# Kernel optimization log

Hardware: AMD Instinct MI355X
Metric: run time of the kernel (lower is better)

## Reference

```python
import jax, jax.numpy as jnp
import numpy as np

L, D, H, G = 3, 64, 4, 64            # layers, hidden_dim, heads, num_graphs
N, E = 20000, 320000                  # nodes, edges
HD = H * D                            # heads * out_channels = 256
DENSE = 256
EPS = 1e-5


def setup_inputs() -> dict:
    key = jax.random.key(0)
    ks = jax.random.split(key, 32)
    s = 0.05
    f32 = jnp.float32
    inp = {
        "x": jax.random.normal(ks[0], (N, D), f32),
        "edge_attr": jax.random.normal(ks[1], (E, D), f32),
        "edge_index": jax.random.randint(ks[2], (2, E), 0, N, dtype=jnp.int32),
        "batch": ((jnp.arange(N, dtype=jnp.int32) * G) // N).astype(jnp.int32),
        # per-layer TransformerConv params (stacked over layer dim)
        "Wq": jax.random.normal(ks[3], (L, D, HD), f32) * s,
        "bq": jnp.zeros((L, HD), f32),
        "Wk": jax.random.normal(ks[4], (L, D, HD), f32) * s,
        "bk": jnp.zeros((L, HD), f32),
        "Wv": jax.random.normal(ks[5], (L, D, HD), f32) * s,
        "bv": jnp.zeros((L, HD), f32),
        "We": jax.random.normal(ks[6], (L, D, HD), f32) * s,   # lin_edge (no bias in PyG)
        "Wskip": jax.random.normal(ks[7], (L, D, HD), f32) * s,
        "bskip": jnp.zeros((L, HD), f32),
        "bn_gamma": jnp.ones((L, HD), f32),
        "bn_beta": jnp.zeros((L, HD), f32),
        "Wt": jax.random.normal(ks[8], (L, HD, D), f32) * s,   # transf_layers
        "bt": jnp.zeros((L, D), f32),
        # MLP head
        "W1": jax.random.normal(ks[9], (2 * D, DENSE), f32) * s,
        "b1": jnp.zeros((DENSE,), f32),
        "W2": jax.random.normal(ks[10], (DENSE, DENSE // 2), f32) * s,
        "b2": jnp.zeros((DENSE // 2,), f32),
        "W3": jax.random.normal(ks[11], (DENSE // 2, 1), f32) * s,
        "b3": jnp.zeros((1,), f32),
    }
    return inp


def _transformer_conv(x, edge_attr, src, dst, Wq, bq, Wk, bk, Wv, bv, We, Wskip, bskip):
    # PyG TransformerConv, concat=True, beta=False, root_weight=True, eval (no attn dropout)
    q = (x @ Wq + bq).reshape(N, H, D)[dst]                 # [E,H,C]
    k = (x @ Wk + bk).reshape(N, H, D)[src]                 # [E,H,C]
    v = (x @ Wv + bv).reshape(N, H, D)[src]                 # [E,H,C]
    e = (edge_attr @ We).reshape(E, H, D)                   # [E,H,C]
    k = k + e
    logits = (q * k).sum(-1) / jnp.sqrt(jnp.asarray(D, x.dtype))  # [E,H]
    m = jax.ops.segment_max(logits, dst, num_segments=N)    # stable softmax per dst node
    p = jnp.exp(logits - m[dst])
    z = jax.ops.segment_sum(p, dst, num_segments=N)
    w = p / z[dst]                                          # [E,H]
    msg = w[..., None] * (v + e)                            # [E,H,C]
    agg = jax.ops.segment_sum(msg, dst, num_segments=N).reshape(N, HD)
    return agg + x @ Wskip + bskip                          # [N, H*C]


def _batchnorm(h, gamma, beta):
    mu = h.mean(0)
    var = h.var(0)  # biased, as torch BN uses for normalization
    return (h - mu) * jax.lax.rsqrt(var + EPS) * gamma + beta


def reference(x, edge_attr, edge_index, batch, Wq, bq, Wk, bk, Wv, bv, We, Wskip,
              bskip, bn_gamma, bn_beta, Wt, bt, W1, b1, W2, b2, W3, b3):
    src, dst = edge_index[0], edge_index[1]
    counts = jax.ops.segment_sum(jnp.ones((N,), x.dtype), batch, num_segments=G)
    rep = jnp.zeros((G, 2 * D), x.dtype)
    for i in range(L):
        h = _transformer_conv(x, edge_attr, src, dst, Wq[i], bq[i], Wk[i], bk[i],
                              Wv[i], bv[i], We[i], Wskip[i], bskip[i])
        h = _batchnorm(h, bn_gamma[i], bn_beta[i])
        x = jax.nn.relu(h @ Wt[i] + bt[i])                  # [N, D]
        gmx = jax.ops.segment_max(x, batch, num_segments=G)
        gav = jax.ops.segment_sum(x, batch, num_segments=G) / counts[:, None]
        rep = rep + jnp.concatenate([gmx, gav], axis=1)     # sum of per-layer reps
    out = jax.nn.relu(rep @ W1 + b1)
    out = jax.nn.relu(out @ W2 + b2)
    return out @ W3 + b3                                    # [G, 1]
```

## Files before the change

### kernel.cpp

```cpp
#include <hip/hip_runtime.h>
#include <math.h>
#include <float.h>

#define N_NODES 20000
#define N_PAD 20032
#define N_EDGES 320000
#define NGRAPH 64
#define NLAYER 3
#define BN_EPS 1e-5f

typedef short bf16x8 __attribute__((ext_vector_type(8)));
typedef float f32x4 __attribute__((ext_vector_type(4)));
typedef unsigned short u16x8 __attribute__((ext_vector_type(8)));

__device__ inline unsigned short f2bf(float f) {
    unsigned int u = __float_as_uint(f);
    unsigned int r = u + 0x7FFF + ((u >> 16) & 1);
    return (unsigned short)(r >> 16);
}
__device__ inline float bf2f(unsigned short s) {
    return __uint_as_float((unsigned int)s << 16);
}

__global__ void count_kernel(const int* __restrict__ ei, int* __restrict__ cnt) {
    int e = blockIdx.x * blockDim.x + threadIdx.x;
    if (e < N_EDGES) atomicAdd(&cnt[ei[N_EDGES + e]], 1);
}

__global__ void scan_kernel(const int* __restrict__ cnt, int* __restrict__ rowptr) {
    __shared__ int sh[256];
    int t = threadIdx.x;
    const int CH = (N_NODES + 255) / 256;
    int base = t * CH;
    int s = 0;
    for (int i = 0; i < CH; i++) { int idx = base + i; if (idx < N_NODES) s += cnt[idx]; }
    sh[t] = s;
    __syncthreads();
    for (int off = 1; off < 256; off <<= 1) {
        int v = sh[t];
        int add = (t >= off) ? sh[t - off] : 0;
        __syncthreads();
        sh[t] = v + add;
        __syncthreads();
    }
    int run = sh[t] - s;
    for (int i = 0; i < CH; i++) {
        int idx = base + i;
        if (idx < N_NODES) { rowptr[idx] = run; run += cnt[idx]; }
    }
    if (t == 255) rowptr[N_NODES] = sh[255];
}

__global__ void fill_kernel(const int* __restrict__ ei, const int* __restrict__ rowptr,
                            int* __restrict__ cur, int* __restrict__ eidx,
                            int* __restrict__ esrc) {
    int e = blockIdx.x * blockDim.x + threadIdx.x;
    if (e < N_EDGES) {
        int dst = ei[N_EDGES + e];
        int pos = atomicAdd(&cur[dst], 1);
        int slot = rowptr[dst] + pos;
        eidx[slot] = e;
        esrc[slot] = ei[e];
    }
}

__global__ void permute_ea_b_kernel(const float* __restrict__ edge_attr,
                                    const int* __restrict__ eidx,
                                    unsigned short* __restrict__ eaPb) {
    int idx = blockIdx.x * blockDim.x + threadIdx.x;
    if (idx < N_EDGES * 16) {
        int j = idx >> 4, c4 = idx & 15;
        float4 v = *(const float4*)(edge_attr + (size_t)eidx[j] * 64 + c4 * 4);
        ((ushort4*)eaPb)[idx] = make_ushort4(f2bf(v.x), f2bf(v.y), f2bf(v.z), f2bf(v.w));
    }
}

__global__ void wallt2_kernel(const float* __restrict__ Wq, const float* __restrict__ Wk,
                              const float* __restrict__ Wv, const float* __restrict__ Ws,
                              const float* __restrict__ We,
                              const float* __restrict__ bq, const float* __restrict__ bk,
                              const float* __restrict__ bv, const float* __restrict__ bs,
                              unsigned short* __restrict__ WallT, float* __restrict__ ball) {
    int c = blockIdx.x, l = blockIdx.y, k = threadIdx.x;
    int seg = c >> 8, ci = c & 255;
    if (seg < 4) {
        const float* W; const float* b;
        switch (seg) {
            case 0:  W = Wq; b = bq; break;
            case 1:  W = Wk; b = bk; break;
            case 2:  W = Wv; b = bv; break;
            default: W = Ws; b = bs; break;
        }
        WallT[(size_t)l * 81920 + c * 64 + k] = f2bf(W[l * 16384 + k * 256 + ci]);
        if (k == 0) ball[l * 1280 + c] = b[l * 256 + ci];
    } else {
        int h = ci >> 6, d = ci & 63;
        const float* Wql = Wq + l * 16384;
        const float* Wel = We + l * 16384;
        float acc = 0.f;
        for (int cc = 0; cc < 64; cc++)
            acc += Wql[k * 256 + h * 64 + cc] * Wel[d * 256 + h * 64 + cc];
        WallT[(size_t)l * 81920 + c * 64 + k] = f2bf(acc);
        if (k == 0) {
            const float* bql = bq + l * 256;
            float ab = 0.f;
            for (int cc = 0; cc < 64; cc++) ab += bql[h * 64 + cc] * Wel[d * 256 + h * 64 + cc];
            ball[l * 1280 + c] = ab;
        }
    }
}

__global__ void xtobf_kernel(const float* __restrict__ x, unsigned short* __restrict__ xbf) {
    int i4 = blockIdx.x * 256 + threadIdx.x;
    if (i4 >= N_PAD * 64 / 4) return;
    int n = i4 >> 4;
    ushort4 o;
    if (n < N_NODES) {
        float4 v = ((const float4*)x)[i4];
        o = make_ushort4(f2bf(v.x), f2bf(v.y), f2bf(v.z), f2bf(v.w));
    } else o = make_ushort4(0, 0, 0, 0);
    ((ushort4*)xbf)[i4] = o;
}

__global__ __launch_bounds__(256) void gemm_qkvsu3_kernel(
    const unsigned short* __restrict__ xbf,
    const unsigned short* __restrict__ WallT,
    const float* __restrict__ ball,
    unsigned short* __restrict__ qbf, unsigned short* __restrict__ kvbf,
    unsigned short* __restrict__ sbf, unsigned short* __restrict__ ubf) {
    int t = threadIdx.x, wid = t >> 6, lane = t & 63;
    int lrow = lane & 15, lk = lane >> 4;

    bf16x8 bfrag[2][4][2];
    float bias[2][4];
    unsigned short* outp[2]; int ostr[2], mul[2], obase[2];
#pragma unroll
    for (int cg = 0; cg < 2; cg++) {
        int ys = blockIdx.y * 2 + cg;
        int col0 = ys * 64;
        int q = ys & 3;
        if (ys < 4)       { outp[cg] = qbf;  ostr[cg] = 256; mul[cg] = 1; obase[cg] = q * 64; }
        else if (ys < 8)  { outp[cg] = kvbf; ostr[cg] = 512; mul[cg] = 2; obase[cg] = q * 128; }
        else if (ys < 12) { outp[cg] = kvbf; ostr[cg] = 512; mul[cg] = 2; obase[cg] = q * 128 + 1; }
        else if (ys < 16) { outp[cg] = sbf;  ostr[cg] = 256; mul[cg] = 1; obase[cg] = q * 64; }
        else              { outp[cg] = ubf;  ostr[cg] = 256; mul[cg] = 1; obase[cg] = q * 64; }
#pragma unroll
        for (int ct = 0; ct < 4; ct++) {
#pragma unroll
            for (int kc = 0; kc < 2; kc++)
                bfrag[cg][ct][kc] = *(const bf16x8*)(WallT +
                    (size_t)(col0 + ct * 16 + lrow) * 64 + kc * 32 + lk * 8);
            bias[cg][ct] = ball[col0 + ct * 16 + lrow];
        }
    }

    for (int nc = blockIdx.x; nc < N_PAD / 64; nc += gridDim.x) {
        int n0 = nc * 64 + wid * 16;
        bf16x8 a0 = *(const bf16x8*)(xbf + (size_t)(n0 + lrow) * 64 + lk * 8);
        bf16x8 a1 = *(const bf16x8*)(xbf + (size_t)(n0 + lrow) * 64 + 32 + lk * 8);
#pragma unroll
        for (int cg = 0; cg < 2; cg++) {
#pragma unroll
            for (int ct = 0; ct < 4; ct++) {
                f32x4 acc = {bias[cg][ct], bias[cg][ct], bias[cg][ct], bias[cg][ct]};
                acc = __builtin_amdgcn_mfma_f32_16x16x32_bf16(a0, bfrag[cg][ct][0], acc, 0, 0, 0);
                acc = __builtin_amdgcn_mfma_f32_16x16x32_bf16(a1, bfrag[cg][ct][1], acc, 0, 0, 0);
                int cl = ct * 16 + lrow;
#pragma unroll
                for (int r = 0; r < 4; r++) {
                    int n = n0 + lk * 4 + r;
                    if (n < N_NODES)
                        outp[cg][(size_t)n * ostr[cg] + obase[cg] + cl * mul[cg]] = f2bf(acc[r]);
                }
            }
        }
    }
}

__global__ __launch_bounds__(256) void attn8_kernel(
    const unsigned short* __restrict__ eaPb,
    const float* __restrict__ ea_f32,
    const int* __restrict__ eaidx,
    const int* __restrict__ rowptr, const int* __restrict__ esrc,
    const unsigned short* __restrict__ qbf, const unsigned short* __restrict__ ubf,
    const unsigned short* __restrict__ kvbf,
    const unsigned short* __restrict__ sbf,
    unsigned short* __restrict__ hskb,
    unsigned short* __restrict__ raccb) {
    int t = threadIdx.x;
    int wid = t >> 6, lane = t & 63;
    int c4 = lane * 4;
    int ec4 = (lane & 15) * 4;
    for (int n = blockIdx.x * 4 + wid; n < N_NODES; n += gridDim.x * 4) {
        ushort4 qu = *(const ushort4*)(qbf + (size_t)n * 256 + c4);
        ushort4 uu = *(const ushort4*)(ubf + (size_t)n * 256 + c4);
        float4 q4 = make_float4(bf2f(qu.x), bf2f(qu.y), bf2f(qu.z), bf2f(qu.w));
        float4 u4 = make_float4(bf2f(uu.x), bf2f(uu.y), bf2f(uu.z), bf2f(uu.w));
        int j0 = rowptr[n];
        int cnt = rowptr[n + 1] - j0;
        float l = 0.f;
        float4 a4 = make_float4(0.f, 0.f, 0.f, 0.f), r4 = a4;
        u16x8 kvA = {0, 0, 0, 0, 0, 0, 0, 0}, kvB = kvA;
        float4 eA = make_float4(0.f, 0.f, 0.f, 0.f), eB = eA;

#define LOADE(KV, EV, JJ) do { \
        int _j = j0 + (JJ); \
        int _s = __builtin_amdgcn_readfirstlane(esrc[_j]); \
        KV = *(const u16x8*)(kvbf + (size_t)_s * 512 + c4 * 2); \
        if (eaPb) { ushort4 _e = *(const ushort4*)(eaPb + (size_t)_j * 64 + ec4); \
                    EV = make_float4(bf2f(_e.x), bf2f(_e.y), bf2f(_e.z), bf2f(_e.w)); } \
        else { EV = *(const float4*)(ea_f32 + (size_t)eaidx[_j] * 64 + ec4); } \
    } while (0)

#define PROC(KV, EV) do { \
        float p = q4.x * bf2f(KV[0]) + q4.y * bf2f(KV[2]) \
                + q4.z * bf2f(KV[4]) + q4.w * bf2f(KV[6]) \
                + u4.x * EV.x + u4.y * EV.y + u4.z * EV.z + u4.w * EV.w; \
        p += __shfl_xor(p, 1); p += __shfl_xor(p, 2); \
        p += __shfl_xor(p, 4); p += __shfl_xor(p, 8); \
        p = __expf(p * 0.125f); \
        l += p; \
        a4.x += p * bf2f(KV[1]); a4.y += p * bf2f(KV[3]); \
        a4.z += p * bf2f(KV[5]); a4.w += p * bf2f(KV[7]); \
        r4.x += p * EV.x; r4.y += p * EV.y; r4.z += p * EV.z; r4.w += p * EV.w; \
    } while (0)

        if (cnt > 0) LOADE(kvA, eA, 0);
        if (cnt > 1) LOADE(kvB, eB, 1);
        int jj = 0;
        for (; jj + 1 < cnt; jj += 2) {
            u16x8 kv0 = kvA; float4 e0 = eA;
            if (jj + 2 < cnt) LOADE(kvA, eA, jj + 2);
            PROC(kv0, e0);
            u16x8 kv1 = kvB; float4 e1 = eB;
            if (jj + 3 < cnt) LOADE(kvB, eB, jj + 3);
            PROC(kv1, e1);
        }
        if (jj < cnt) PROC(kvA, eA);
#undef LOADE
#undef PROC
        float inv = (l > 0.f) ? 1.f / l : 0.f;
        ushort4 su = *(const ushort4*)(sbf + (size_t)n * 256 + c4);
        *(ushort4*)(hskb + (size_t)n * 256 + c4) = make_ushort4(
            f2bf(a4.x * inv + bf2f(su.x)), f2bf(a4.y * inv + bf2f(su.y)),
            f2bf(a4.z * inv + bf2f(su.z)), f2bf(a4.w * inv + bf2f(su.w)));
        *(ushort4*)(raccb + (size_t)n * 256 + c4) = make_ushort4(
            f2bf(r4.x * inv), f2bf(r4.y * inv), f2bf(r4.z * inv), f2bf(r4.w * inv));
    }
}

__global__ __launch_bounds__(256) void msgbn2_kernel(
    const unsigned short* __restrict__ raccb, const float* __restrict__ We,
    const unsigned short* __restrict__ hskb, unsigned short* __restrict__ hbf,
    float* __restrict__ statsL) {
    int t = threadIdx.x;
    float wcol[64];
#pragma unroll
    for (int d = 0; d < 64; d++) wcol[d] = We[d * 256 + t];
    int hoff = t & 192;
    float s = 0.f, s2 = 0.f;
    for (int n = blockIdx.x * 4; n < N_NODES; n += gridDim.x * 4) {
#pragma unroll
        for (int ni = 0; ni < 4; ni++) {
            const unsigned short* rrow = raccb + (size_t)(n + ni) * 256 + hoff;
            float acc = 0.f;
#pragma unroll
            for (int d4 = 0; d4 < 64; d4 += 4) {
                ushort4 r4 = *(const ushort4*)(rrow + d4);
                acc += bf2f(r4.x) * wcol[d4] + bf2f(r4.y) * wcol[d4 + 1]
                     + bf2f(r4.z) * wcol[d4 + 2] + bf2f(r4.w) * wcol[d4 + 3];
            }
            float hv = bf2f(hskb[(size_t)(n + ni) * 256 + t]) + acc;
            hbf[(size_t)(n + ni) * 256 + t] = f2bf(hv);
            s += hv; s2 += hv * hv;
        }
    }
    int base = (blockIdx.x & 7) * 512;
    atomicAdd(&statsL[base + t], s);
    atomicAdd(&statsL[base + 256 + t], s2);
}

__global__ __launch_bounds__(256) void bn_fold5_kernel(
    const float* __restrict__ statsL,
    const float* __restrict__ gamma, const float* __restrict__ beta,
    const float* __restrict__ Wt, const float* __restrict__ bt,
    unsigned short* __restrict__ WtpT,
    float* __restrict__ biasp) {
    __shared__ float aL[256], bbL[256], part[256];
    int t = threadIdx.x;
    float sum = 0.f, sq = 0.f;
#pragma unroll
    for (int s = 0; s < 8; s++) {
        sum += statsL[s * 512 + t];
        sq  += statsL[s * 512 + 256 + t];
    }
    float mean = sum * (1.f / N_NODES);
    float var = sq * (1.f / N_NODES) - mean * mean;
    float a = rsqrtf(var + BN_EPS) * gamma[t];
    aL[t] = a;
    bbL[t] = beta[t] - mean * a;
    __syncthreads();
    int i0 = blockIdx.x * 2048;
    for (int i = i0 + t; i < i0 + 2048; i += 256) {
        int k = i >> 6, o = i & 63;
        WtpT[o * 256 + k] = f2bf(aL[k] * Wt[i]);
    }
    if (blockIdx.x == 0) {
        float p = 0.f;
        int o = t & 63, kq = (t >> 6) * 64;
        for (int kk = kq; kk < kq + 64; kk++) p += bbL[kk] * Wt[kk * 64 + o];
        part[t] = p;
        __syncthreads();
        if (t < 64) biasp[t] = bt[t] + part[t] + part[64 + t] + part[128 + t] + part[192 + t];
    }
}

__global__ __launch_bounds__(256) void xform4_kernel(
    const unsigned short* __restrict__ hbf,
    const unsigned short* __restrict__ WtpT,
    const float* __restrict__ biasp,
    unsigned short* __restrict__ xbf,
    float* __restrict__ poolmx, float* __restrict__ poolsm, int layer) {
    __shared__ float xt[64][65];
    __shared__ float red[4][2][2][64];
    int t = threadIdx.x, wid = t >> 6, lane = t & 63;
    int lrow = lane & 15, lk = lane >> 4;
    bf16x8 bfrag[4][8];
#pragma unroll
    for (int ct = 0; ct < 4; ct++)
#pragma unroll
        for (int kc = 0; kc < 8; kc++)
            bfrag[ct][kc] = *(const bf16x8*)(WtpT +
                (size_t)(ct * 16 + lrow) * 256 + kc * 32 + lk * 8);
    float bias[4];
#pragma unroll
    for (int ct = 0; ct < 4; ct++) bias[ct] = biasp[ct * 16 + lrow];

    for (int nc = blockIdx.x; nc < N_PAD / 64; nc += gridDim.x) {
        int n0 = nc * 64;
        int nw = n0 + wid * 16;
        f32x4 acc[4];
#pragma unroll
        for (int ct = 0; ct < 4; ct++)
            acc[ct] = {bias[ct], bias[ct], bias[ct], bias[ct]};
#pragma unroll
        for (int kc = 0; kc < 8; kc++) {
            bf16x8 a = *(const bf16x8*)(hbf + (size_t)(nw + lrow) * 256 + kc * 32 + lk * 8);
#pragma unroll
            for (int ct = 0; ct < 4; ct++)
                acc[ct] = __builtin_amdgcn_mfma_f32_16x16x32_bf16(a, bfrag[ct][kc], acc[ct], 0, 0, 0);
        }
#pragma unroll
        for (int ct = 0; ct < 4; ct++) {
            int c = ct * 16 + lrow;
#pragma unroll
            for (int r = 0; r < 4; r++) {
                int n = nw + lk * 4 + r;
                float v = fmaxf(acc[ct][r], 0.f);
                xt[wid * 16 + lk * 4 + r][c] = v;
                if (n < N_NODES) xbf[(size_t)n * 64 + c] = f2bf(v);
            }
        }
        __syncthreads();
        int g0 = (n0 * 64) / 20000;
        int b = ((20000 * (g0 + 1) + 63) >> 6) - n0;
        if (b > 64) b = 64;
        {
            int ch = t & 63, rp = t >> 6;
            float mx0 = 0.f, sm0 = 0.f, mx1 = 0.f, sm1 = 0.f;
            for (int r = rp * 16; r < rp * 16 + 16; r++) {
                if (n0 + r < N_NODES) {
                    float v = xt[r][ch];
                    if (r < b) { mx0 = fmaxf(mx0, v); sm0 += v; }
                    else       { mx1 = fmaxf(mx1, v); sm1 += v; }
                }
            }
            red[rp][0][0][ch] = mx0; red[rp][0][1][ch] = sm0;
            red[rp][1][0][ch] = mx1; red[rp][1][1][ch] = sm1;
        }
        __syncthreads();
        if (t < 128) {
            int seg = t >> 6, ch = t & 63;
            float m = red[0][seg][0][ch], s = red[0][seg][1][ch];
#pragma unroll
            for (int w = 1; w < 4; w++) {
                m = fmaxf(m, red[w][seg][0][ch]);
                s += red[w][seg][1][ch];
            }
            int g = g0 + seg;
            bool valid = (seg == 0) || (b < 64 && g < NGRAPH);
            if (valid) {
                atomicMax((unsigned int*)&poolmx[(layer * NGRAPH + g) * 64 + ch],
                          __float_as_uint(m));
                atomicAdd(&poolsm[(layer * NGRAPH + g) * 64 + ch], s);
            }
        }
        __syncthreads();
    }
}

__global__ __launch_bounds__(256) void head_kernel(
    const float* __restrict__ poolmx, const float* __restrict__ poolsm,
    const float* __restrict__ W1, const float* __restrict__ b1,
    const float* __restrict__ W2, const float* __restrict__ b2,
    const float* __restrict__ W3, const float* __restrict__ b3,
    float* __restrict__ out) {
    int g = blockIdx.x, t = threadIdx.x;
    __shared__ float repL[128], o1sh[256], o2sh[128];
    if (t < 128) {
        int d = t & 63;
        int start = (N_NODES * g + 63) >> 6;
        int end = (N_NODES * (g + 1) + 63) >> 6;
        float v = 0.f;
        if (t < 64) {
#pragma unroll
            for (int l = 0; l < NLAYER; l++) v += poolmx[(l * NGRAPH + g) * 64 + d];
        } else {
            float inv = 1.f / (float)(end - start);
#pragma unroll
            for (int l = 0; l < NLAYER; l++) v += poolsm[(l * NGRAPH + g) * 64 + d] * inv;
        }
        repL[t] = v;
    }
    __syncthreads();
    float a1 = b1[t];
    for (int k = 0; k < 128; k++) a1 += repL[k] * W1[k * 256 + t];
    o1sh[t] = fmaxf(a1, 0.f);
    __syncthreads();
    if (t < 128) {
        float a2 = b2[t];
        for (int k = 0; k < 256; k++) a2 += o1sh[k] * W2[k * 128 + t];
        o2sh[t] = fmaxf(a2, 0.f);
    }
    __syncthreads();
    if (t < 64) {
        float p = o2sh[t] * W3[t] + o2sh[t + 64] * W3[t + 64];
#pragma unroll
        for (int off = 32; off; off >>= 1) p += __shfl_xor(p, off);
        if (t == 0) out[g] = p + b3[0];
    }
}

extern "C" void kernel_launch(void* const* d_in, const int* in_sizes, int n_in,
                              void* d_out, int out_size, void* d_ws, size_t ws_size,
                              hipStream_t stream) {
    const float* x         = (const float*)d_in[0];
    const float* edge_attr = (const float*)d_in[1];
    const int*   ei        = (const int*)d_in[2];
    const float* Wq  = (const float*)d_in[4];
    const float* bq  = (const float*)d_in[5];
    const float* Wk  = (const float*)d_in[6];
    const float* bk  = (const float*)d_in[7];
    const float* Wv  = (const float*)d_in[8];
    const float* bv  = (const float*)d_in[9];
    const float* We  = (const float*)d_in[10];
    const float* Wsk = (const float*)d_in[11];
    const float* bsk = (const float*)d_in[12];
    const float* gam = (const float*)d_in[13];
    const float* bet = (const float*)d_in[14];
    const float* Wt  = (const float*)d_in[15];
    const float* bt  = (const float*)d_in[16];
    const float* W1  = (const float*)d_in[17];
    const float* b1  = (const float*)d_in[18];
    const float* W2  = (const float*)d_in[19];
    const float* b2  = (const float*)d_in[20];
    const float* W3  = (const float*)d_in[21];
    const float* b3  = (const float*)d_in[22];
    float* out = (float*)d_out;

    char* ws = (char*)d_ws;
    size_t off = 0;
    auto alloc = [&](size_t bytes) -> char* {
        char* p = ws + off;
        off += (bytes + 255) & ~(size_t)255;
        return p;
    };
    int*   rowptr = (int*)alloc((N_NODES + 1) * sizeof(int));
    int*   eidx   = (int*)alloc((size_t)N_EDGES * sizeof(int));
    int*   esrc   = (int*)alloc(((size_t)N_EDGES + 16) * sizeof(int));
    unsigned short* qbf  = (unsigned short*)alloc((size_t)N_NODES * 256 * 2);
    unsigned short* kvbf = (unsigned short*)alloc((size_t)N_NODES * 512 * 2);
    unsigned short* sbf  = (unsigned short*)alloc((size_t)N_NODES * 256 * 2);
    unsigned short* ubf  = (unsigned short*)alloc((size_t)N_NODES * 256 * 2);
    unsigned short* hskb = (unsigned short*)alloc((size_t)N_NODES * 256 * 2);
    unsigned short* raccb= (unsigned short*)alloc((size_t)N_NODES * 256 * 2);
    unsigned short* hbf  = (unsigned short*)alloc((size_t)N_PAD * 256 * 2);
    unsigned short* xbf  = (unsigned short*)alloc((size_t)N_PAD * 64 * 2);
    unsigned short* WtpT = (unsigned short*)alloc(64 * 256 * 2);
    float* biasp  = (float*)alloc(64 * sizeof(float));
    unsigned short* WallT = (unsigned short*)alloc((size_t)NLAYER * 81920 * 2);
    float* ball   = (float*)alloc((size_t)NLAYER * 1280 * sizeof(float));
    size_t zero_off = off;
    int*   cur1   = (int*)alloc(N_NODES * sizeof(int));
    int*   cur2   = (int*)alloc(N_NODES * sizeof(int));
    float* statsA = (float*)alloc((size_t)NLAYER * 8 * 512 * sizeof(float));
    float* poolmx = (float*)alloc((size_t)NLAYER * NGRAPH * 64 * sizeof(float));
    float* poolsm = (float*)alloc((size_t)NLAYER * NGRAPH * 64 * sizeof(float));
    size_t zero_bytes = off - zero_off;
    unsigned short* eaPb = (unsigned short*)alloc((size_t)N_EDGES * 64 * 2);
    bool perm = (off <= ws_size);

    hipMemsetAsync(ws + zero_off, 0, zero_bytes, stream);

    count_kernel<<<(N_EDGES + 255) / 256, 256, 0, stream>>>(ei, cur1);
    scan_kernel<<<1, 256, 0, stream>>>(cur1, rowptr);
    fill_kernel<<<(N_EDGES + 255) / 256, 256, 0, stream>>>(ei, rowptr, cur2, eidx, esrc);
    if (perm) {
        permute_ea_b_kernel<<<(N_EDGES * 16 + 255) / 256, 256, 0, stream>>>(
            edge_attr, eidx, eaPb);
    }

    wallt2_kernel<<<dim3(1280, NLAYER), 64, 0, stream>>>(
        Wq, Wk, Wv, Wsk, We, bq, bk, bv, bsk, WallT, ball);
    xtobf_kernel<<<(N_PAD * 64 / 4 + 255) / 256, 256, 0, stream>>>(x, xbf);

    for (int i = 0; i < NLAYER; i++) {
        gemm_qkvsu3_kernel<<<dim3(79, 10), 256, 0, stream>>>(
            xbf, WallT + (size_t)i * 81920, ball + i * 1280, qbf, kvbf, sbf, ubf);

        attn8_kernel<<<5000, 256, 0, stream>>>(
            perm ? eaPb : (const unsigned short*)nullptr, edge_attr,
            eidx, rowptr, esrc, qbf, ubf, kvbf, sbf, hskb, raccb);

        msgbn2_kernel<<<1250, 256, 0, stream>>>(
            raccb, We + i * 16384, hskb, hbf, statsA + (size_t)i * 4096);

        bn_fold5_kernel<<<8, 256, 0, stream>>>(
            statsA + (size_t)i * 4096, gam + i * 256, bet + i * 256,
            Wt + i * 16384, bt + i * 64, WtpT, biasp);

        xform4_kernel<<<157, 256, 0, stream>>>(
            hbf, WtpT, biasp, xbf, poolmx, poolsm, i);
    }

    head_kernel<<<64, 256, 0, stream>>>(poolmx, poolsm, W1, b1, W2, b2, W3, b3, out);
}
```

Measured before the change: 663.3 us.

## Store K/V in fp8 and fuse BN fold into xform kernel

The QKV GEMM now writes the gathered K and V tensors as interleaved fp8 bytes instead of bf16, and the attention kernel decodes them with fp8 conversion intrinsics. This halves the bytes per random gather in the edge loop, at the cost of lower precision in the attention logits and values. The separate BN-fold launch is folded into the xform kernel, where each block recomputes the scale, bias and scaled weight fragments itself. This removes one launch per layer but repeats that small amount of work in every block. The attention grid is also halved.

```diff
diff --git a/kernel.cpp b/kernel.cpp
--- a/kernel.cpp
+++ b/kernel.cpp
@@ -11,7 +11,6 @@
 
 typedef short bf16x8 __attribute__((ext_vector_type(8)));
 typedef float f32x4 __attribute__((ext_vector_type(4)));
-typedef unsigned short u16x8 __attribute__((ext_vector_type(8)));
 
 __device__ inline unsigned short f2bf(float f) {
     unsigned int u = __float_as_uint(f);
@@ -122,28 +121,29 @@
     ((ushort4*)xbf)[i4] = o;
 }
 
-__global__ __launch_bounds__(256) void gemm_qkvsu3_kernel(
+__global__ __launch_bounds__(256) void gemm_qkvsu4_kernel(
     const unsigned short* __restrict__ xbf,
     const unsigned short* __restrict__ WallT,
     const float* __restrict__ ball,
-    unsigned short* __restrict__ qbf, unsigned short* __restrict__ kvbf,
+    unsigned short* __restrict__ qbf, unsigned char* __restrict__ kvf8,
     unsigned short* __restrict__ sbf, unsigned short* __restrict__ ubf) {
     int t = threadIdx.x, wid = t >> 6, lane = t & 63;
     int lrow = lane & 15, lk = lane >> 4;
 
     bf16x8 bfrag[2][4][2];
     float bias[2][4];
-    unsigned short* outp[2]; int ostr[2], mul[2], obase[2];
+    int kind[2];
+    unsigned short* outb[2]; int obase[2];
 #pragma unroll
     for (int cg = 0; cg < 2; cg++) {
         int ys = blockIdx.y * 2 + cg;
         int col0 = ys * 64;
         int q = ys & 3;
-        if (ys < 4)       { outp[cg] = qbf;  ostr[cg] = 256; mul[cg] = 1; obase[cg] = q * 64; }
-        else if (ys < 8)  { outp[cg] = kvbf; ostr[cg] = 512; mul[cg] = 2; obase[cg] = q * 128; }
-        else if (ys < 12) { outp[cg] = kvbf; ostr[cg] = 512; mul[cg] = 2; obase[cg] = q * 128 + 1; }
-        else if (ys < 16) { outp[cg] = sbf;  ostr[cg] = 256; mul[cg] = 1; obase[cg] = q * 64; }
-        else              { outp[cg] = ubf;  ostr[cg] = 256; mul[cg] = 1; obase[cg] = q * 64; }
+        if (ys < 4)       { kind[cg] = 0; outb[cg] = qbf; obase[cg] = q * 64; }
+        else if (ys < 8)  { kind[cg] = 1; outb[cg] = nullptr; obase[cg] = q * 64; }
+        else if (ys < 12) { kind[cg] = 2; outb[cg] = nullptr; obase[cg] = q * 64; }
+        else if (ys < 16) { kind[cg] = 0; outb[cg] = sbf; obase[cg] = q * 64; }
+        else              { kind[cg] = 0; outb[cg] = ubf; obase[cg] = q * 64; }
 #pragma unroll
         for (int ct = 0; ct < 4; ct++) {
 #pragma unroll
@@ -169,21 +169,30 @@
 #pragma unroll
                 for (int r = 0; r < 4; r++) {
                     int n = n0 + lk * 4 + r;
-                    if (n < N_NODES)
-                        outp[cg][(size_t)n * ostr[cg] + obase[cg] + cl * mul[cg]] = f2bf(acc[r]);
+                    if (n < N_NODES) {
+                        if (kind[cg] == 0) {
+                            outb[cg][(size_t)n * 256 + obase[cg] + cl] = f2bf(acc[r]);
+                        } else {
+                            unsigned int pk = __builtin_amdgcn_cvt_pk_fp8_f32(
+                                acc[r], acc[r], 0, false);
+                            int ch = obase[cg] + cl;
+                            kvf8[(size_t)n * 512 + 2 * ch + (kind[cg] - 1)] =
+                                (unsigned char)pk;
+                        }
+                    }
                 }
             }
         }
     }
 }
 
-__global__ __launch_bounds__(256) void attn8_kernel(
+__global__ __launch_bounds__(256) void attn9_kernel(
     const unsigned short* __restrict__ eaPb,
     const float* __restrict__ ea_f32,
     const int* __restrict__ eaidx,
     const int* __restrict__ rowptr, const int* __restrict__ esrc,
     const unsigned short* __restrict__ qbf, const unsigned short* __restrict__ ubf,
-    const unsigned short* __restrict__ kvbf,
+    const unsigned char* __restrict__ kvf8,
     const unsigned short* __restrict__ sbf,
     unsigned short* __restrict__ hskb,
     unsigned short* __restrict__ raccb) {
@@ -200,28 +209,34 @@
         int cnt = rowptr[n + 1] - j0;
         float l = 0.f;
         float4 a4 = make_float4(0.f, 0.f, 0.f, 0.f), r4 = a4;
-        u16x8 kvA = {0, 0, 0, 0, 0, 0, 0, 0}, kvB = kvA;
+        uint2 kvA = make_uint2(0, 0), kvB = kvA;
         float4 eA = make_float4(0.f, 0.f, 0.f, 0.f), eB = eA;
 
 #define LOADE(KV, EV, JJ) do { \
         int _j = j0 + (JJ); \
         int _s = __builtin_amdgcn_readfirstlane(esrc[_j]); \
-        KV = *(const u16x8*)(kvbf + (size_t)_s * 512 + c4 * 2); \
+        KV = *(const uint2*)(kvf8 + (size_t)_s * 512 + c4 * 2); \
         if (eaPb) { ushort4 _e = *(const ushort4*)(eaPb + (size_t)_j * 64 + ec4); \
                     EV = make_float4(bf2f(_e.x), bf2f(_e.y), bf2f(_e.z), bf2f(_e.w)); } \
         else { EV = *(const float4*)(ea_f32 + (size_t)eaidx[_j] * 64 + ec4); } \
     } while (0)
 
 #define PROC(KV, EV) do { \
-        float p = q4.x * bf2f(KV[0]) + q4.y * bf2f(KV[2]) \
-                + q4.z * bf2f(KV[4]) + q4.w * bf2f(KV[6]) \
+        float K0 = __builtin_amdgcn_cvt_f32_fp8(KV.x, 0); \
+        float V0 = __builtin_amdgcn_cvt_f32_fp8(KV.x, 1); \
+        float K1 = __builtin_amdgcn_cvt_f32_fp8(KV.x, 2); \
+        float V1 = __builtin_amdgcn_cvt_f32_fp8(KV.x, 3); \
+        float K2 = __builtin_amdgcn_cvt_f32_fp8(KV.y, 0); \
+        float V2 = __builtin_amdgcn_cvt_f32_fp8(KV.y, 1); \
+        float K3 = __builtin_amdgcn_cvt_f32_fp8(KV.y, 2); \
+        float V3 = __builtin_amdgcn_cvt_f32_fp8(KV.y, 3); \
+        float p = q4.x * K0 + q4.y * K1 + q4.z * K2 + q4.w * K3 \
                 + u4.x * EV.x + u4.y * EV.y + u4.z * EV.z + u4.w * EV.w; \
         p += __shfl_xor(p, 1); p += __shfl_xor(p, 2); \
         p += __shfl_xor(p, 4); p += __shfl_xor(p, 8); \
         p = __expf(p * 0.125f); \
         l += p; \
-        a4.x += p * bf2f(KV[1]); a4.y += p * bf2f(KV[3]); \
-        a4.z += p * bf2f(KV[5]); a4.w += p * bf2f(KV[7]); \
+        a4.x += p * V0; a4.y += p * V1; a4.z += p * V2; a4.w += p * V3; \
         r4.x += p * EV.x; r4.y += p * EV.y; r4.z += p * EV.z; r4.w += p * EV.w; \
     } while (0)
 
@@ -229,10 +244,10 @@
         if (cnt > 1) LOADE(kvB, eB, 1);
         int jj = 0;
         for (; jj + 1 < cnt; jj += 2) {
-            u16x8 kv0 = kvA; float4 e0 = eA;
+            uint2 kv0 = kvA; float4 e0 = eA;
             if (jj + 2 < cnt) LOADE(kvA, eA, jj + 2);
             PROC(kv0, e0);
-            u16x8 kv1 = kvB; float4 e1 = eB;
+            uint2 kv1 = kvB; float4 e1 = eB;
             if (jj + 3 < cnt) LOADE(kvB, eB, jj + 3);
             PROC(kv1, e1);
         }
@@ -280,61 +295,62 @@
     atomicAdd(&statsL[base + 256 + t], s2);
 }
 
-__global__ __launch_bounds__(256) void bn_fold5_kernel(
+__global__ __launch_bounds__(256) void xform5_kernel(
+    const unsigned short* __restrict__ hbf,
+    const float* __restrict__ Wt,
+    const float* __restrict__ gamma, const float* __restrict__ beta,
+    const float* __restrict__ bt,
     const float* __restrict__ statsL,
-    const float* __restrict__ gamma, const float* __restrict__ beta,
-    const float* __restrict__ Wt, const float* __restrict__ bt,
-    unsigned short* __restrict__ WtpT,
-    float* __restrict__ biasp) {
-    __shared__ float aL[256], bbL[256], part[256];
-    int t = threadIdx.x;
-    float sum = 0.f, sq = 0.f;
-#pragma unroll
-    for (int s = 0; s < 8; s++) {
-        sum += statsL[s * 512 + t];
-        sq  += statsL[s * 512 + 256 + t];
-    }
-    float mean = sum * (1.f / N_NODES);
-    float var = sq * (1.f / N_NODES) - mean * mean;
-    float a = rsqrtf(var + BN_EPS) * gamma[t];
-    aL[t] = a;
-    bbL[t] = beta[t] - mean * a;
-    __syncthreads();
-    int i0 = blockIdx.x * 2048;
-    for (int i = i0 + t; i < i0 + 2048; i += 256) {
-        int k = i >> 6, o = i & 63;
-        WtpT[o * 256 + k] = f2bf(aL[k] * Wt[i]);
-    }
-    if (blockIdx.x == 0) {
-        float p = 0.f;
-        int o = t & 63, kq = (t >> 6) * 64;
-        for (int kk = kq; kk < kq + 64; kk++) p += bbL[kk] * Wt[kk * 64 + o];
-        part[t] = p;
-        __syncthreads();
-        if (t < 64) biasp[t] = bt[t] + part[t] + part[64 + t] + part[128 + t] + part[192 + t];
-    }
-}
-
-__global__ __launch_bounds__(256) void xform4_kernel(
-    const unsigned short* __restrict__ hbf,
-    const unsigned short* __restrict__ WtpT,
-    const float* __restrict__ biasp,
     unsigned short* __restrict__ xbf,
     float* __restrict__ poolmx, float* __restrict__ poolsm, int layer) {
     __shared__ float xt[64][65];
     __shared__ float red[4][2][2][64];
+    __shared__ float aL[256], bbL[256], partb[256], biasL[64];
     int t = threadIdx.x, wid = t >> 6, lane = t & 63;
     int lrow = lane & 15, lk = lane >> 4;
+
+    {
+        float sum = 0.f, sq = 0.f;
+#pragma unroll
+        for (int s = 0; s < 8; s++) {
+            sum += statsL[s * 512 + t];
+            sq  += statsL[s * 512 + 256 + t];
+        }
+        float mean = sum * (1.f / N_NODES);
+        float var = sq * (1.f / N_NODES) - mean * mean;
+        float a = rsqrtf(var + BN_EPS) * gamma[t];
+        aL[t] = a;
+        bbL[t] = beta[t] - mean * a;
+    }
+    __syncthreads();
+    {
+        float p = 0.f;
+        int o = t & 63, kq = (t >> 6) * 64;
+        for (int kk = kq; kk < kq + 64; kk++) p += bbL[kk] * Wt[kk * 64 + o];
+        partb[t] = p;
+    }
+    __syncthreads();
+    if (t < 64) biasL[t] = bt[t] + partb[t] + partb[64 + t] + partb[128 + t] + partb[192 + t];
+    __syncthreads();
+
     bf16x8 bfrag[4][8];
 #pragma unroll
-    for (int ct = 0; ct < 4; ct++)
-#pragma unroll
-        for (int kc = 0; kc < 8; kc++)
-            bfrag[ct][kc] = *(const bf16x8*)(WtpT +
-                (size_t)(ct * 16 + lrow) * 256 + kc * 32 + lk * 8);
+    for (int ct = 0; ct < 4; ct++) {
+        int o = ct * 16 + lrow;
+#pragma unroll
+        for (int kc = 0; kc < 8; kc++) {
+            short tmp[8];
+#pragma unroll
+            for (int i = 0; i < 8; i++) {
+                int k = kc * 32 + lk * 8 + i;
+                tmp[i] = (short)f2bf(aL[k] * Wt[k * 64 + o]);
+            }
+            bfrag[ct][kc] = *(bf16x8*)tmp;
+        }
+    }
     float bias[4];
 #pragma unroll
-    for (int ct = 0; ct < 4; ct++) bias[ct] = biasp[ct * 16 + lrow];
+    for (int ct = 0; ct < 4; ct++) bias[ct] = biasL[ct * 16 + lrow];
 
     for (int nc = blockIdx.x; nc < N_PAD / 64; nc += gridDim.x) {
         int n0 = nc * 64;
@@ -479,15 +495,13 @@
     int*   eidx   = (int*)alloc((size_t)N_EDGES * sizeof(int));
     int*   esrc   = (int*)alloc(((size_t)N_EDGES + 16) * sizeof(int));
     unsigned short* qbf  = (unsigned short*)alloc((size_t)N_NODES * 256 * 2);
-    unsigned short* kvbf = (unsigned short*)alloc((size_t)N_NODES * 512 * 2);
+    unsigned char*  kvf8 = (unsigned char*)alloc((size_t)N_NODES * 512);
     unsigned short* sbf  = (unsigned short*)alloc((size_t)N_NODES * 256 * 2);
     unsigned short* ubf  = (unsigned short*)alloc((size_t)N_NODES * 256 * 2);
     unsigned short* hskb = (unsigned short*)alloc((size_t)N_NODES * 256 * 2);
     unsigned short* raccb= (unsigned short*)alloc((size_t)N_NODES * 256 * 2);
     unsigned short* hbf  = (unsigned short*)alloc((size_t)N_PAD * 256 * 2);
     unsigned short* xbf  = (unsigned short*)alloc((size_t)N_PAD * 64 * 2);
-    unsigned short* WtpT = (unsigned short*)alloc(64 * 256 * 2);
-    float* biasp  = (float*)alloc(64 * sizeof(float));
     unsigned short* WallT = (unsigned short*)alloc((size_t)NLAYER * 81920 * 2);
     float* ball   = (float*)alloc((size_t)NLAYER * 1280 * sizeof(float));
     size_t zero_off = off;
@@ -515,22 +529,19 @@
     xtobf_kernel<<<(N_PAD * 64 / 4 + 255) / 256, 256, 0, stream>>>(x, xbf);
 
     for (int i = 0; i < NLAYER; i++) {
-        gemm_qkvsu3_kernel<<<dim3(79, 10), 256, 0, stream>>>(
-            xbf, WallT + (size_t)i * 81920, ball + i * 1280, qbf, kvbf, sbf, ubf);
-
-        attn8_kernel<<<5000, 256, 0, stream>>>(
+        gemm_qkvsu4_kernel<<<dim3(79, 10), 256, 0, stream>>>(
+            xbf, WallT + (size_t)i * 81920, ball + i * 1280, qbf, kvf8, sbf, ubf);
+
+        attn9_kernel<<<2500, 256, 0, stream>>>(
             perm ? eaPb : (const unsigned short*)nullptr, edge_attr,
-            eidx, rowptr, esrc, qbf, ubf, kvbf, sbf, hskb, raccb);
+            eidx, rowptr, esrc, qbf, ubf, kvf8, sbf, hskb, raccb);
 
         msgbn2_kernel<<<1250, 256, 0, stream>>>(
             raccb, We + i * 16384, hskb, hbf, statsA + (size_t)i * 4096);
 
-        bn_fold5_kernel<<<8, 256, 0, stream>>>(
-            statsA + (size_t)i * 4096, gam + i * 256, bet + i * 256,
-            Wt + i * 16384, bt + i * 64, WtpT, biasp);
-
-        xform4_kernel<<<157, 256, 0, stream>>>(
-            hbf, WtpT, biasp, xbf, poolmx, poolsm, i);
+        xform5_kernel<<<157, 256, 0, stream>>>(
+            hbf, Wt + i * 16384, gam + i * 256, bet + i * 256, bt + i * 64,
+            statsA + (size_t)i * 4096, xbf, poolmx, poolsm, i);
     }
 
     head_kernel<<<64, 256, 0, stream>>>(poolmx, poolsm, W1, b1, W2, b2, W3, b3, out);
```

Measured after the change: 630.6 us. 4.9% less time.
